# Optimization experiments

Measured on AMD Instinct MI355X. Metric: run time of the kernel, lower is better.

Reference implementation:

```python
import jax, jax.numpy as jnp
import numpy as np

B, T, I, H, C, S = 512, 128, 512, 512, 97, 26  # batch, enc_len, input, hidden, classes, num_steps


def setup_inputs() -> dict:
    key = jax.random.key(0)
    ks = jax.random.split(key, 12)
    s = 0.05
    d = {}
    d["batch_H"] = jax.random.normal(ks[0], (B, T, I), dtype=jnp.float32)
    d["text"] = jax.random.randint(ks[1], (B, S), 0, C)
    # attention cell params
    d["W_feat"] = jax.random.normal(ks[2], (H, I), dtype=jnp.float32) * s   # feature_projection (no bias)
    d["W_hid"] = jax.random.normal(ks[3], (H, H), dtype=jnp.float32) * s    # hidden_projection
    d["b_hid"] = jnp.zeros((H,), dtype=jnp.float32)
    d["w_score"] = jax.random.normal(ks[4], (H,), dtype=jnp.float32) * s    # attention_score (Linear(H,1), no bias)
    # LSTMCell params, PyTorch gate order [i, f, g, o]
    d["W_ih"] = jax.random.normal(ks[5], (4 * H, I + C), dtype=jnp.float32) * s
    d["W_hh"] = jax.random.normal(ks[6], (4 * H, H), dtype=jnp.float32) * s
    d["b_ih"] = jnp.zeros((4 * H,), dtype=jnp.float32)
    d["b_hh"] = jnp.zeros((4 * H,), dtype=jnp.float32)
    # generator
    d["W_gen"] = jax.random.normal(ks[7], (C, H), dtype=jnp.float32) * s
    d["b_gen"] = jnp.zeros((C,), dtype=jnp.float32)
    return d


def reference(batch_H, text, W_feat, W_hid, b_hid, w_score, W_ih, W_hh, b_ih, b_hh, W_gen, b_gen):
    Bb, Tt, _ = batch_H.shape
    Hh = W_hid.shape[0]
    Cc = W_gen.shape[0]
    # step-invariant: project encoder features once  [B, T, H]
    feat = jnp.einsum('bti,hi->bth', batch_H, W_feat)
    onehots = jax.nn.one_hot(text, Cc, dtype=batch_H.dtype)  # [B, S, C]

    def step(carry, oh):
        h, c = carry
        hp = h @ W_hid.T + b_hid                                     # [B, H]
        e = jnp.einsum('bth,h->bt', jnp.tanh(feat + hp[:, None, :]), w_score)
        alpha = jax.nn.softmax(e, axis=1)                            # [B, T]
        ctx = jnp.einsum('bt,bti->bi', alpha, batch_H)               # [B, I]
        x = jnp.concatenate([ctx, oh], axis=1)                       # [B, I+C]
        gates = x @ W_ih.T + b_ih + h @ W_hh.T + b_hh                # [B, 4H]
        i_g, f_g, g_g, o_g = jnp.split(gates, 4, axis=1)
        c2 = jax.nn.sigmoid(f_g) * c + jax.nn.sigmoid(i_g) * jnp.tanh(g_g)
        h2 = jax.nn.sigmoid(o_g) * jnp.tanh(c2)
        return (h2, c2), h2

    init = (jnp.zeros((Bb, Hh), dtype=batch_H.dtype), jnp.zeros((Bb, Hh), dtype=batch_H.dtype))
    _, hs = jax.lax.scan(step, init, jnp.swapaxes(onehots, 0, 1))    # hs: [S, B, H]
    out_h = jnp.swapaxes(hs, 0, 1)                                   # [B, S, H]
    probs = out_h @ W_gen.T + b_gen                                  # [B, S, C]
    return probs
```

## Files before the change

### kernel.cpp

```cpp
#include <hip/hip_runtime.h>
#include <hip/hip_bf16.h>
#include <stdint.h>
#include <stddef.h>

typedef __bf16 bf16;
typedef __bf16 v8bf __attribute__((ext_vector_type(8)));
typedef float  v4f  __attribute__((ext_vector_type(4)));

#define B_ 512
#define T_ 128
#define I_ 512
#define H_ 512
#define C_ 97
#define S_ 26

__device__ __forceinline__ void async_copy16(void* lds, const void* g) {
  __builtin_amdgcn_global_load_lds((__attribute__((address_space(1))) void*)g,
                                   (__attribute__((address_space(3))) void*)lds,
                                   16, 0, 0);
}

__device__ __forceinline__ float fast_tanh(float x) {
  float e = __expf(2.0f * x);
  return fmaf(-2.0f, __builtin_amdgcn_rcpf(e + 1.0f), 1.0f);
}
__device__ __forceinline__ float fast_sigmoid(float x) {
  float t = __expf(-x);
  return __builtin_amdgcn_rcpf(1.0f + t);
}

__device__ __forceinline__ void zero_acc(v4f acc[4][4]) {
  v4f z = {0.f, 0.f, 0.f, 0.f};
#pragma unroll
  for (int i = 0; i < 4; ++i)
#pragma unroll
    for (int j = 0; j < 4; ++j) acc[i][j] = z;
}

template <int KTOT>
__device__ __forceinline__ void mm_db32(const bf16* aRow0, const bf16* aRow1,
                                        const bf16* bRow0, const bf16* bRow1,
                                        bf16* As, bf16* Bs, int tid,
                                        v4f acc[4][4]) {
  constexpr int NT = KTOT / 32;
  const int wave = tid >> 6, lane = tid & 63;
  const int wr = (wave >> 1) * 64, wc = (wave & 1) * 64;
  const int fr = lane & 15, fq = lane >> 4;
  const int s0 = tid * 8;
  const int aBase = (wr + fr) * 32 + fq * 8;
  const int bBase = (wc + fr) * 32 + fq * 8;
  async_copy16(As + s0, aRow0);
  async_copy16(As + s0 + 2048, aRow1);
  async_copy16(Bs + s0, bRow0);
  async_copy16(Bs + s0 + 2048, bRow1);
  __syncthreads();
#pragma unroll 2
  for (int t = 0; t < NT; ++t) {
    const int cb = (t & 1) << 12;
    if (t + 1 < NT) {
      const int nb = 4096 - cb;
      const int kk = (t + 1) * 32;
      async_copy16(As + nb + s0, aRow0 + kk);
      async_copy16(As + nb + s0 + 2048, aRow1 + kk);
      async_copy16(Bs + nb + s0, bRow0 + kk);
      async_copy16(Bs + nb + s0 + 2048, bRow1 + kk);
    }
    v8bf av[4], bv[4];
#pragma unroll
    for (int i = 0; i < 4; ++i) av[i] = *(const v8bf*)(As + cb + aBase + i * 512);
#pragma unroll
    for (int j = 0; j < 4; ++j) bv[j] = *(const v8bf*)(Bs + cb + bBase + j * 512);
#pragma unroll
    for (int i = 0; i < 4; ++i) {
#pragma unroll
      for (int j = 0; j < 4; ++j) {
        acc[i][j] = __builtin_amdgcn_mfma_f32_16x16x32_bf16(av[i], bv[j], acc[i][j], 0, 0, 0);
      }
    }
    __syncthreads();
  }
}

template <int KTOT>
__device__ __forceinline__ void mm_db64(const bf16* aRow0, const bf16* aRow1,
                                        const bf16* bRow0, const bf16* bRow1,
                                        bf16* As, bf16* Bs, int tid,
                                        v4f acc[4][4]) {
  constexpr int NT = KTOT / 64;
  const int wave = tid >> 6, lane = tid & 63;
  const int wr = (wave >> 1) * 64, wc = (wave & 1) * 64;
  const int fr = lane & 15, fq = lane >> 4;
  const int s0 = tid * 8;
  const int aBase = (wr + fr) * 32 + fq * 8;
  const int bBase = (wc + fr) * 32 + fq * 8;
#define STAGE64(buf, kk)                                          \
  do {                                                            \
    async_copy16(As + (buf) + s0, aRow0 + (kk));                  \
    async_copy16(As + (buf) + s0 + 2048, aRow1 + (kk));           \
    async_copy16(As + (buf) + s0 + 4096, aRow0 + (kk) + 32);      \
    async_copy16(As + (buf) + s0 + 6144, aRow1 + (kk) + 32);      \
    async_copy16(Bs + (buf) + s0, bRow0 + (kk));                  \
    async_copy16(Bs + (buf) + s0 + 2048, bRow1 + (kk));           \
    async_copy16(Bs + (buf) + s0 + 4096, bRow0 + (kk) + 32);      \
    async_copy16(Bs + (buf) + s0 + 6144, bRow1 + (kk) + 32);      \
  } while (0)
  STAGE64(0, 0);
  __syncthreads();
#pragma unroll 2
  for (int t = 0; t < NT; ++t) {
    const int cb = (t & 1) << 13;
    if (t + 1 < NT) STAGE64(8192 - cb, (t + 1) * 64);
#pragma unroll
    for (int ks = 0; ks < 2; ++ks) {
      const int sb = cb + ks * 4096;
      v8bf av[4], bv[4];
#pragma unroll
      for (int i = 0; i < 4; ++i) av[i] = *(const v8bf*)(As + sb + aBase + i * 512);
#pragma unroll
      for (int j = 0; j < 4; ++j) bv[j] = *(const v8bf*)(Bs + sb + bBase + j * 512);
#pragma unroll
      for (int i = 0; i < 4; ++i) {
#pragma unroll
        for (int j = 0; j < 4; ++j) {
          acc[i][j] = __builtin_amdgcn_mfma_f32_16x16x32_bf16(av[i], bv[j], acc[i][j], 0, 0, 0);
        }
      }
    }
    __syncthreads();
  }
#undef STAGE64
}

template <int KTOT>
__device__ __forceinline__ void mm_reg_f32a(const float* aR0, const float* aR1,
                                            const bf16* bRow0, const bf16* bRow1,
                                            bf16* As, bf16* Bs, int tid,
                                            v4f acc[4][4]) {
  const int wave = tid >> 6, lane = tid & 63;
  const int wr = (wave >> 1) * 64, wc = (wave & 1) * 64;
  const int fr = lane & 15, fq = lane >> 4;
  bf16* a_s0 = As + tid * 8;
  bf16* a_s1 = As + (tid + 256) * 8;
  bf16* b_s0 = Bs + tid * 8;
  bf16* b_s1 = Bs + (tid + 256) * 8;
  const bf16* aF[4];
  const bf16* bF[4];
#pragma unroll
  for (int i = 0; i < 4; ++i) {
    aF[i] = As + (wr + i * 16 + fr) * 32 + fq * 8;
    bF[i] = Bs + (wc + i * 16 + fr) * 32 + fq * 8;
  }
  for (int kk = 0; kk < KTOT; kk += 32) {
    v8bf va0, va1;
    const float* p0 = aR0 + kk;
    const float* p1 = aR1 + kk;
    v4f f00 = ((const v4f*)p0)[0], f01 = ((const v4f*)p0)[1];
    v4f f10 = ((const v4f*)p1)[0], f11 = ((const v4f*)p1)[1];
#pragma unroll
    for (int j = 0; j < 4; ++j) {
      va0[j] = (bf16)f00[j]; va0[j + 4] = (bf16)f01[j];
      va1[j] = (bf16)f10[j]; va1[j + 4] = (bf16)f11[j];
    }
    v8bf vb0 = *(const v8bf*)(bRow0 + kk);
    v8bf vb1 = *(const v8bf*)(bRow1 + kk);
    __syncthreads();
    *(v8bf*)a_s0 = va0;
    *(v8bf*)a_s1 = va1;
    *(v8bf*)b_s0 = vb0;
    *(v8bf*)b_s1 = vb1;
    __syncthreads();
    v8bf av[4], bv[4];
#pragma unroll
    for (int i = 0; i < 4; ++i) av[i] = *(const v8bf*)aF[i];
#pragma unroll
    for (int j = 0; j < 4; ++j) bv[j] = *(const v8bf*)bF[j];
#pragma unroll
    for (int i = 0; i < 4; ++i) {
#pragma unroll
      for (int j = 0; j < 4; ++j) {
        acc[i][j] = __builtin_amdgcn_mfma_f32_16x16x32_bf16(av[i], bv[j], acc[i][j], 0, 0, 0);
      }
    }
  }
  __syncthreads();
}

__global__ void k_cvt(const float* __restrict__ src, bf16* __restrict__ dst, int n) {
  int i = (blockIdx.x * 256 + threadIdx.x) * 4;
  if (i + 3 < n) {
    v4f f = *(const v4f*)(src + i);
#pragma unroll
    for (int j = 0; j < 4; ++j) dst[i + j] = (bf16)f[j];
  }
}

__global__ void k_repack(const float* __restrict__ Wih, const float* __restrict__ Whh,
                         bf16* __restrict__ Wcat) {
  int n = blockIdx.x;
  int t = threadIdx.x;
#pragma unroll
  for (int j = 0; j < 4; ++j) {
    int k = t * 4 + j;
    float v = (k < 512) ? Wih[(size_t)n * 609 + k] : Whh[(size_t)n * 512 + (k - 512)];
    Wcat[(size_t)n * 1024 + k] = (bf16)v;
  }
}

__global__ void k_prep_gen(const float* __restrict__ Wg, bf16* __restrict__ Wgen16) {
  int row = blockIdx.x;
  int t = threadIdx.x;
#pragma unroll
  for (int j = 0; j < 2; ++j) {
    int k = t * 2 + j;
    float v = (row < C_) ? Wg[(size_t)row * 512 + k] : 0.0f;
    Wgen16[(size_t)row * 512 + k] = (bf16)v;
  }
}

__global__ void k_prep_oht(const float* __restrict__ Wih, float* __restrict__ OHT) {
  int n = blockIdx.x * 256 + threadIdx.x;
  const float* src = Wih + (size_t)n * 609 + 512;
  for (int c = 0; c < C_; ++c) OHT[(size_t)c * 2048 + n] = src[c];
}


__global__ __launch_bounds__(256, 3) void k_feat16(const bf16* __restrict__ A,
                                                   const bf16* __restrict__ Bw,
                                                   bf16* __restrict__ F) {
  __shared__ bf16 As[2 * 4096];
  __shared__ bf16 Bs[2 * 4096];
  const int tid = threadIdx.x;
  const int m0 = blockIdx.x * 128, n0 = blockIdx.y * 128;
  const int r0 = tid >> 2, k0 = (tid & 3) * 8;
  const bf16* aRow0 = A + (size_t)(m0 + r0) * 512 + k0;
  const bf16* aRow1 = A + (size_t)(m0 + r0 + 64) * 512 + k0;
  const bf16* bRow0 = Bw + (size_t)(n0 + r0) * 512 + k0;
  const bf16* bRow1 = Bw + (size_t)(n0 + r0 + 64) * 512 + k0;
  v4f acc[4][4];
  zero_acc(acc);
  mm_db32<512>(aRow0, aRow1, bRow0, bRow1, As, Bs, tid, acc);
  const int wave = tid >> 6, lane = tid & 63;
  const int wr = (wave >> 1) * 64, wc = (wave & 1) * 64;
  const int fr = lane & 15, fq = lane >> 4;
#pragma unroll
  for (int i = 0; i < 4; ++i) {
#pragma unroll
    for (int j = 0; j < 4; ++j) {
      int col = n0 + wc + j * 16 + fr;
#pragma unroll
      for (int r = 0; r < 4; ++r) {
        int row = m0 + wr + i * 16 + fq * 4 + r;
        F[(size_t)row * 512 + col] = (bf16)acc[i][j][r];
      }
    }
  }
}

__global__ __launch_bounds__(256, 2) void k_feat32(const float* __restrict__ A,
                                                   const bf16* __restrict__ Bw,
                                                   bf16* __restrict__ F) {
  __shared__ bf16 As[128 * 32];
  __shared__ bf16 Bs[128 * 32];
  const int tid = threadIdx.x;
  const int m0 = blockIdx.x * 128, n0 = blockIdx.y * 128;
  const int r0 = tid >> 2, k0 = (tid & 3) * 8;
  const float* aRow0 = A + (size_t)(m0 + r0) * 512 + k0;
  const float* aRow1 = A + (size_t)(m0 + r0 + 64) * 512 + k0;
  const bf16* bRow0 = Bw + (size_t)(n0 + r0) * 512 + k0;
  const bf16* bRow1 = Bw + (size_t)(n0 + r0 + 64) * 512 + k0;
  v4f acc[4][4];
  zero_acc(acc);
  mm_reg_f32a<512>(aRow0, aRow1, bRow0, bRow1, As, Bs, tid, acc);
  const int wave = tid >> 6, lane = tid & 63;
  const int wr = (wave >> 1) * 64, wc = (wave & 1) * 64;
  const int fr = lane & 15, fq = lane >> 4;
#pragma unroll
  for (int i = 0; i < 4; ++i) {
#pragma unroll
    for (int j = 0; j < 4; ++j) {
      int col = n0 + wc + j * 16 + fr;
#pragma unroll
      for (int r = 0; r < 4; ++r) {
        int row = m0 + wr + i * 16 + fq * 4 + r;
        F[(size_t)row * 512 + col] = (bf16)acc[i][j][r];
      }
    }
  }
}

__global__ __launch_bounds__(256) void k_hp(const bf16* __restrict__ xb_cur,
                                            const bf16* __restrict__ Whid16,
                                            const float* __restrict__ b_hid,
                                            float* __restrict__ P) {
  __shared__ bf16 As[2 * 2048];
  __shared__ bf16 Bs[2 * 2048];
  const int tid = threadIdx.x, wave = tid >> 6, lane = tid & 63;
  const int m0 = blockIdx.x * 64, n0 = blockIdx.y * 64;
  const int r0 = tid >> 2, k0 = (tid & 3) * 8;
  const bf16* aRow = xb_cur + (size_t)(m0 + r0) * 1024 + 512 + k0;
  const bf16* bRow = Whid16 + (size_t)(n0 + r0) * 512 + k0;
  const int s0 = tid * 8;
  const int fr = lane & 15, fq = lane >> 4;
  const int aBase = fr * 32 + fq * 8;
  const int bBase = (wave * 16 + fr) * 32 + fq * 8;
  v4f acc[4];
  v4f z = {0.f, 0.f, 0.f, 0.f};
#pragma unroll
  for (int i = 0; i < 4; ++i) acc[i] = z;
  async_copy16(As + s0, aRow);
  async_copy16(Bs + s0, bRow);
  __syncthreads();
#pragma unroll 2
  for (int t = 0; t < 16; ++t) {
    const int cb = (t & 1) << 11;
    if (t + 1 < 16) {
      const int nb = 2048 - cb;
      const int kk = (t + 1) * 32;
      async_copy16(As + nb + s0, aRow + kk);
      async_copy16(Bs + nb + s0, bRow + kk);
    }
    v8bf bv = *(const v8bf*)(Bs + cb + bBase);
#pragma unroll
    for (int i = 0; i < 4; ++i) {
      acc[i] = __builtin_amdgcn_mfma_f32_16x16x32_bf16(*(const v8bf*)(As + cb + aBase + i * 512),
                                                       bv, acc[i], 0, 0, 0);
    }
    __syncthreads();
  }
  const int col = n0 + wave * 16 + fr;
  const float bh = b_hid[col];
#pragma unroll
  for (int i = 0; i < 4; ++i) {
#pragma unroll
    for (int r = 0; r < 4; ++r) {
      int row = m0 + i * 16 + fq * 4 + r;
      P[(size_t)row * 512 + col] = acc[i][r] + bh;
    }
  }
}

template <bool CTX16>
__global__ __launch_bounds__(512, 4) void k_attn(const bf16* __restrict__ F,
                                                 const float* __restrict__ P,
                                                 const float* __restrict__ w_score,
                                                 const void* __restrict__ bHv,
                                                 bf16* __restrict__ xb_cur) {
  const int b = blockIdx.x;
  const int tid = threadIdx.x, wave = tid >> 6, lane = tid & 63;
  __shared__ float e_s[T_];
  __shared__ float alpha_s[T_];
  __shared__ float red[8][I_];
  float Pv[8], Wv[8];
  {
    const float* p = P + (size_t)b * H_ + lane * 8;
#pragma unroll
    for (int j = 0; j < 8; ++j) Pv[j] = p[j];
    const float* w = w_score + lane * 8;
#pragma unroll
    for (int j = 0; j < 8; ++j) Wv[j] = w[j];
  }
  const bf16* Fb = F + (size_t)b * T_ * H_ + lane * 8;
#pragma unroll
  for (int t = wave; t < T_; t += 32) {
    v8bf r0 = *(const v8bf*)(Fb + (size_t)t * H_);
    v8bf r1 = *(const v8bf*)(Fb + (size_t)(t + 8) * H_);
    v8bf r2 = *(const v8bf*)(Fb + (size_t)(t + 16) * H_);
    v8bf r3 = *(const v8bf*)(Fb + (size_t)(t + 24) * H_);
    float a0 = 0.f, a1 = 0.f, a2 = 0.f, a3 = 0.f;
#pragma unroll
    for (int j = 0; j < 8; ++j) a0 = fmaf(Wv[j], fast_tanh((float)r0[j] + Pv[j]), a0);
#pragma unroll
    for (int j = 0; j < 8; ++j) a1 = fmaf(Wv[j], fast_tanh((float)r1[j] + Pv[j]), a1);
#pragma unroll
    for (int j = 0; j < 8; ++j) a2 = fmaf(Wv[j], fast_tanh((float)r2[j] + Pv[j]), a2);
#pragma unroll
    for (int j = 0; j < 8; ++j) a3 = fmaf(Wv[j], fast_tanh((float)r3[j] + Pv[j]), a3);
#pragma unroll
    for (int off = 32; off; off >>= 1) {
      a0 += __shfl_xor(a0, off, 64);
      a1 += __shfl_xor(a1, off, 64);
      a2 += __shfl_xor(a2, off, 64);
      a3 += __shfl_xor(a3, off, 64);
    }
    if (lane == 0) {
      e_s[t] = a0; e_s[t + 8] = a1; e_s[t + 16] = a2; e_s[t + 24] = a3;
    }
  }
  __syncthreads();
  if (wave == 0) {
    float e0 = e_s[lane], e1 = e_s[lane + 64];
    float m = fmaxf(e0, e1);
#pragma unroll
    for (int off = 32; off; off >>= 1) m = fmaxf(m, __shfl_xor(m, off, 64));
    float x0 = __expf(e0 - m), x1 = __expf(e1 - m);
    float ssum = x0 + x1;
#pragma unroll
    for (int off = 32; off; off >>= 1) ssum += __shfl_xor(ssum, off, 64);
    float inv = __builtin_amdgcn_rcpf(ssum);
    alpha_s[lane] = x0 * inv;
    alpha_s[lane + 64] = x1 * inv;
  }
  __syncthreads();
  const int i0 = lane * 8;
  float c[8];
#pragma unroll
  for (int j = 0; j < 8; ++j) c[j] = 0.f;
  if (CTX16) {
    const bf16* hb = (const bf16*)bHv + (size_t)b * T_ * I_ + i0;
#pragma unroll
    for (int t = wave; t < T_; t += 32) {
      float aa0 = alpha_s[t], aa1 = alpha_s[t + 8];
      float aa2 = alpha_s[t + 16], aa3 = alpha_s[t + 24];
      v8bf p0 = *(const v8bf*)(hb + (size_t)t * I_);
      v8bf p1 = *(const v8bf*)(hb + (size_t)(t + 8) * I_);
      v8bf p2 = *(const v8bf*)(hb + (size_t)(t + 16) * I_);
      v8bf p3 = *(const v8bf*)(hb + (size_t)(t + 24) * I_);
#pragma unroll
      for (int j = 0; j < 8; ++j) {
        c[j] = fmaf(aa0, (float)p0[j], c[j]);
        c[j] = fmaf(aa1, (float)p1[j], c[j]);
        c[j] = fmaf(aa2, (float)p2[j], c[j]);
        c[j] = fmaf(aa3, (float)p3[j], c[j]);
      }
    }
  } else {
    const float* hf = (const float*)bHv + (size_t)b * T_ * I_ + i0;
#pragma unroll
    for (int t = wave; t < T_; t += 32) {
      float aa0 = alpha_s[t], aa1 = alpha_s[t + 8];
      float aa2 = alpha_s[t + 16], aa3 = alpha_s[t + 24];
      const float* p0 = hf + (size_t)t * I_;
      const float* p1 = hf + (size_t)(t + 8) * I_;
      const float* p2 = hf + (size_t)(t + 16) * I_;
      const float* p3 = hf + (size_t)(t + 24) * I_;
      v4f q00 = ((const v4f*)p0)[0], q01 = ((const v4f*)p0)[1];
      v4f q10 = ((const v4f*)p1)[0], q11 = ((const v4f*)p1)[1];
      v4f q20 = ((const v4f*)p2)[0], q21 = ((const v4f*)p2)[1];
      v4f q30 = ((const v4f*)p3)[0], q31 = ((const v4f*)p3)[1];
#pragma unroll
      for (int j = 0; j < 4; ++j) {
        c[j]     = fmaf(aa0, q00[j], c[j]);
        c[j + 4] = fmaf(aa0, q01[j], c[j + 4]);
        c[j]     = fmaf(aa1, q10[j], c[j]);
        c[j + 4] = fmaf(aa1, q11[j], c[j + 4]);
        c[j]     = fmaf(aa2, q20[j], c[j]);
        c[j + 4] = fmaf(aa2, q21[j], c[j + 4]);
        c[j]     = fmaf(aa3, q30[j], c[j]);
        c[j + 4] = fmaf(aa3, q31[j], c[j + 4]);
      }
    }
  }
#pragma unroll
  for (int j = 0; j < 8; ++j) red[wave][i0 + j] = c[j];
  __syncthreads();
  {
    int i = tid;
    float s = red[0][i] + red[1][i] + red[2][i] + red[3][i] +
              red[4][i] + red[5][i] + red[6][i] + red[7][i];
    xb_cur[(size_t)b * 1024 + i] = (bf16)s;
  }
}

__global__ __launch_bounds__(256, 2) void k_gates(const bf16* __restrict__ xb_cur,
                                                  const bf16* __restrict__ Wcat,
                                                  const float* __restrict__ OHT,
                                                  const float* __restrict__ b_ih,
                                                  const float* __restrict__ b_hh,
                                                  const int* __restrict__ text,
                                                  float* __restrict__ c_state,
                                                  bf16* __restrict__ out_h,
                                                  bf16* __restrict__ xb_nxt, int s) {
  __shared__ union {
    struct { bf16 A[2 * 8192]; bf16 Bv[2 * 8192]; } st;
    float Cs[128 * 132];
  } sm;
  const int tid = threadIdx.x;
  const int m0 = blockIdx.x * 128;
  const int j0 = blockIdx.y * 32;
  const int r0 = tid >> 2, k0 = (tid & 3) * 8;
  const int nw0 = (r0 >> 5) * 512 + j0 + (r0 & 31);
  const int nw1 = (((r0 + 64) >> 5)) * 512 + j0 + ((r0 + 64) & 31);
  const bf16* aRow0 = xb_cur + (size_t)(m0 + r0) * 1024 + k0;
  const bf16* aRow1 = xb_cur + (size_t)(m0 + r0 + 64) * 1024 + k0;
  const bf16* bRow0 = Wcat + (size_t)nw0 * 1024 + k0;
  const bf16* bRow1 = Wcat + (size_t)nw1 * 1024 + k0;
  v4f acc[4][4];
  zero_acc(acc);
  mm_db64<1024>(aRow0, aRow1, bRow0, bRow1, sm.st.A, sm.st.Bv, tid, acc);
  const int wave = tid >> 6, lane = tid & 63;
  const int wr = (wave >> 1) * 64, wc = (wave & 1) * 64;
  const int fr = lane & 15, fq = lane >> 4;
  int tcv[4][4];
#pragma unroll
  for (int i = 0; i < 4; ++i) {
#pragma unroll
    for (int r = 0; r < 4; ++r) {
      tcv[i][r] = text[(size_t)(m0 + wr + i * 16 + fq * 4 + r) * S_ + s];
    }
  }
#pragma unroll
  for (int j = 0; j < 4; ++j) {
    int cl = wc + j * 16 + fr;
    int nw = (cl >> 5) * 512 + j0 + (cl & 31);
    float bias = b_ih[nw] + b_hh[nw];
    const float* oh = OHT + nw;
#pragma unroll
    for (int i = 0; i < 4; ++i) {
#pragma unroll
      for (int r = 0; r < 4; ++r) {
        int rl = wr + i * 16 + fq * 4 + r;
        sm.Cs[rl * 132 + cl] = acc[i][j][r] + bias + oh[(size_t)tcv[i][r] * 2048];
      }
    }
  }
  __syncthreads();
#pragma unroll
  for (int it = 0; it < 16; ++it) {
    int idx = tid + it * 256;
    int r = idx >> 5, q = idx & 31;
    float ig = sm.Cs[r * 132 + q];
    float fg = sm.Cs[r * 132 + 32 + q];
    float gg = sm.Cs[r * 132 + 64 + q];
    float og = sm.Cs[r * 132 + 96 + q];
    size_t cix = (size_t)(m0 + r) * 512 + j0 + q;
    float c2 = fast_sigmoid(fg) * c_state[cix] + fast_sigmoid(ig) * fast_tanh(gg);
    float h2 = fast_sigmoid(og) * fast_tanh(c2);
    c_state[cix] = c2;
    bf16 hb = (bf16)h2;
    xb_nxt[(size_t)(m0 + r) * 1024 + 512 + j0 + q] = hb;
    out_h[((size_t)(m0 + r) * S_ + s) * 512 + j0 + q] = hb;
  }
}

__global__ __launch_bounds__(256, 2) void k_gen(const bf16* __restrict__ out_h,
                                                const bf16* __restrict__ Wgen16,
                                                const float* __restrict__ b_gen,
                                                float* __restrict__ out) {
  __shared__ bf16 As[2 * 8192];
  __shared__ bf16 Bs[2 * 8192];
  const int tid = threadIdx.x;
  const int m0 = blockIdx.x * 128;
  const int r0 = tid >> 2, k0 = (tid & 3) * 8;
  const bf16* aRow0 = out_h + (size_t)(m0 + r0) * 512 + k0;
  const bf16* aRow1 = out_h + (size_t)(m0 + r0 + 64) * 512 + k0;
  const bf16* bRow0 = Wgen16 + (size_t)r0 * 512 + k0;
  const bf16* bRow1 = Wgen16 + (size_t)(r0 + 64) * 512 + k0;
  v4f acc[4][4];
  zero_acc(acc);
  mm_db64<512>(aRow0, aRow1, bRow0, bRow1, As, Bs, tid, acc);
  const int wave = tid >> 6, lane = tid & 63;
  const int wr = (wave >> 1) * 64, wc = (wave & 1) * 64;
  const int fr = lane & 15, fq = lane >> 4;
#pragma unroll
  for (int i = 0; i < 4; ++i) {
#pragma unroll
    for (int j = 0; j < 4; ++j) {
      int col = wc + j * 16 + fr;
      if (col < C_) {
        float bg = b_gen[col];
#pragma unroll
        for (int r = 0; r < 4; ++r) {
          int row = m0 + wr + i * 16 + fq * 4 + r;
          out[(size_t)row * C_ + col] = acc[i][j][r] + bg;
        }
      }
    }
  }
}

extern "C" void kernel_launch(void* const* d_in, const int* in_sizes, int n_in,
                              void* d_out, int out_size, void* d_ws, size_t ws_size,
                              hipStream_t stream) {
  (void)in_sizes; (void)n_in; (void)out_size;
  const float* batch_H = (const float*)d_in[0];
  const int*   text    = (const int*)d_in[1];
  const float* W_feat  = (const float*)d_in[2];
  const float* W_hid   = (const float*)d_in[3];
  const float* b_hid   = (const float*)d_in[4];
  const float* w_score = (const float*)d_in[5];
  const float* W_ih    = (const float*)d_in[6];
  const float* W_hh    = (const float*)d_in[7];
  const float* b_ih    = (const float*)d_in[8];
  const float* b_hh    = (const float*)d_in[9];
  const float* W_gen   = (const float*)d_in[10];
  const float* b_gen   = (const float*)d_in[11];
  float* out = (float*)d_out;

  char* ws = (char*)d_ws;
  bf16*  F       = (bf16*)(ws);
  bf16*  out_h   = (bf16*)(ws + 67108864);
  float* P       = (float*)(ws + 80740352);
  bf16*  xb0     = (bf16*)(ws + 81788928);
  bf16*  xb1     = (bf16*)(ws + 82837504);
  float* c_state = (float*)(ws + 83886080);
  bf16*  Wcat    = (bf16*)(ws + 84934656);
  bf16*  Wf16    = (bf16*)(ws + 89128960);
  bf16*  Whid16  = (bf16*)(ws + 89653248);
  bf16*  Wgen16  = (bf16*)(ws + 90177536);
  float* OHT     = (float*)(ws + 90308608);
  bf16*  bH16    = (bf16*)(ws + 91357184);
  const bool useBH16 = (ws_size >= (size_t)158466048);

  bf16* xb[2] = {xb0, xb1};

  hipMemsetAsync(xb0, 0, (size_t)512 * 1024 * 2, stream);
  hipMemsetAsync(c_state, 0, (size_t)512 * 512 * 4, stream);

  k_cvt<<<dim3(256), 256, 0, stream>>>(W_feat, Wf16, 512 * 512);
  k_cvt<<<dim3(256), 256, 0, stream>>>(W_hid, Whid16, 512 * 512);
  k_repack<<<dim3(2048), 256, 0, stream>>>(W_ih, W_hh, Wcat);
  k_prep_gen<<<dim3(128), 256, 0, stream>>>(W_gen, Wgen16);
  k_prep_oht<<<dim3(8), 256, 0, stream>>>(W_ih, OHT);

  if (useBH16) {
    k_cvt<<<dim3(32768), 256, 0, stream>>>(batch_H, bH16, B_ * T_ * I_);
    k_feat16<<<dim3(512, 4), 256, 0, stream>>>(bH16, Wf16, F);
  } else {
    k_feat32<<<dim3(512, 4), 256, 0, stream>>>(batch_H, Wf16, F);
  }

  for (int s = 0; s < S_; ++s) {
    bf16* cur = xb[s & 1];
    bf16* nxt = xb[(s + 1) & 1];
    k_hp<<<dim3(8, 8), 256, 0, stream>>>(cur, Whid16, b_hid, P);
    if (useBH16) {
      k_attn<true><<<dim3(512), 512, 0, stream>>>(F, P, w_score, bH16, cur);
    } else {
      k_attn<false><<<dim3(512), 512, 0, stream>>>(F, P, w_score, batch_H, cur);
    }
    k_gates<<<dim3(4, 16), 256, 0, stream>>>(cur, Wcat, OHT, b_ih, b_hh, text,
                                             c_state, out_h, nxt, s);
  }
  k_gen<<<dim3(104, 1), 256, 0, stream>>>(out_h, Wgen16, b_gen, out);
}
```

Baseline: 1.659 ms.

## Replace double-buffered GEMM loops with 4-slot, prefetch-distance-2 pipeline using vmcnt waits

Replaces the double-buffered GEMM mainloops (mm_db32/mm_db64) with a single quad-buffered routine that keeps two K-tiles in flight. Each iteration waits with s_waitcnt vmcnt plus a single barrier, where the old loop used a full __syncthreads after every tile. This is meant to hide more global-load latency in the feat, hidden-projection, gates and generator GEMMs. In exchange the kernels use more LDS, occupancy hints are relaxed, and k_gates drops from K-step 64 to 32 and needs an extra sync before its epilogue reuses shared memory.

```diff
diff --git a/kernel.cpp b/kernel.cpp
--- a/kernel.cpp
+++ b/kernel.cpp
@@ -37,8 +37,15 @@
     for (int j = 0; j < 4; ++j) acc[i][j] = z;
 }
 
+#define WAITBAR(N)                                             \
+  do {                                                         \
+    asm volatile("s_waitcnt vmcnt(" #N ")" ::: "memory");      \
+    __builtin_amdgcn_s_barrier();                              \
+    __builtin_amdgcn_sched_barrier(0);                         \
+  } while (0)
+
 template <int KTOT>
-__device__ __forceinline__ void mm_db32(const bf16* aRow0, const bf16* aRow1,
+__device__ __forceinline__ void mm_qb32(const bf16* aRow0, const bf16* aRow1,
                                         const bf16* bRow0, const bf16* bRow1,
                                         bf16* As, bf16* Bs, int tid,
                                         v4f acc[4][4]) {
@@ -47,29 +54,33 @@
   const int wr = (wave >> 1) * 64, wc = (wave & 1) * 64;
   const int fr = lane & 15, fq = lane >> 4;
   const int s0 = tid * 8;
-  const int aBase = (wr + fr) * 32 + fq * 8;
-  const int bBase = (wc + fr) * 32 + fq * 8;
-  async_copy16(As + s0, aRow0);
-  async_copy16(As + s0 + 2048, aRow1);
-  async_copy16(Bs + s0, bRow0);
-  async_copy16(Bs + s0 + 2048, bRow1);
-  __syncthreads();
-#pragma unroll 2
+  const int aB = (wr + fr) * 32 + fq * 8;
+  const int bB = (wc + fr) * 32 + fq * 8;
+#define STG32(bi, kk)                                   \
+  do {                                                  \
+    const int o = (bi) * 4096 + s0;                     \
+    async_copy16(As + o, aRow0 + (kk));                 \
+    async_copy16(As + o + 2048, aRow1 + (kk));          \
+    async_copy16(Bs + o, bRow0 + (kk));                 \
+    async_copy16(Bs + o + 2048, bRow1 + (kk));          \
+  } while (0)
+  STG32(0, 0);
+  STG32(1, 32);
   for (int t = 0; t < NT; ++t) {
-    const int cb = (t & 1) << 12;
-    if (t + 1 < NT) {
-      const int nb = 4096 - cb;
-      const int kk = (t + 1) * 32;
-      async_copy16(As + nb + s0, aRow0 + kk);
-      async_copy16(As + nb + s0 + 2048, aRow1 + kk);
-      async_copy16(Bs + nb + s0, bRow0 + kk);
-      async_copy16(Bs + nb + s0 + 2048, bRow1 + kk);
-    }
+    if (t + 2 < NT) {
+      STG32((t + 2) & 3, (t + 2) * 32);
+      WAITBAR(8);
+    } else if (t + 1 < NT) {
+      WAITBAR(4);
+    } else {
+      WAITBAR(0);
+    }
+    const int cb = (t & 3) * 4096;
     v8bf av[4], bv[4];
 #pragma unroll
-    for (int i = 0; i < 4; ++i) av[i] = *(const v8bf*)(As + cb + aBase + i * 512);
-#pragma unroll
-    for (int j = 0; j < 4; ++j) bv[j] = *(const v8bf*)(Bs + cb + bBase + j * 512);
+    for (int i = 0; i < 4; ++i) av[i] = *(const v8bf*)(As + cb + aB + i * 512);
+#pragma unroll
+    for (int j = 0; j < 4; ++j) bv[j] = *(const v8bf*)(Bs + cb + bB + j * 512);
 #pragma unroll
     for (int i = 0; i < 4; ++i) {
 #pragma unroll
@@ -77,58 +88,8 @@
         acc[i][j] = __builtin_amdgcn_mfma_f32_16x16x32_bf16(av[i], bv[j], acc[i][j], 0, 0, 0);
       }
     }
-    __syncthreads();
-  }
-}
-
-template <int KTOT>
-__device__ __forceinline__ void mm_db64(const bf16* aRow0, const bf16* aRow1,
-                                        const bf16* bRow0, const bf16* bRow1,
-                                        bf16* As, bf16* Bs, int tid,
-                                        v4f acc[4][4]) {
-  constexpr int NT = KTOT / 64;
-  const int wave = tid >> 6, lane = tid & 63;
-  const int wr = (wave >> 1) * 64, wc = (wave & 1) * 64;
-  const int fr = lane & 15, fq = lane >> 4;
-  const int s0 = tid * 8;
-  const int aBase = (wr + fr) * 32 + fq * 8;
-  const int bBase = (wc + fr) * 32 + fq * 8;
-#define STAGE64(buf, kk)                                          \
-  do {                                                            \
-    async_copy16(As + (buf) + s0, aRow0 + (kk));                  \
-    async_copy16(As + (buf) + s0 + 2048, aRow1 + (kk));           \
-    async_copy16(As + (buf) + s0 + 4096, aRow0 + (kk) + 32);      \
-    async_copy16(As + (buf) + s0 + 6144, aRow1 + (kk) + 32);      \
-    async_copy16(Bs + (buf) + s0, bRow0 + (kk));                  \
-    async_copy16(Bs + (buf) + s0 + 2048, bRow1 + (kk));           \
-    async_copy16(Bs + (buf) + s0 + 4096, bRow0 + (kk) + 32);      \
-    async_copy16(Bs + (buf) + s0 + 6144, bRow1 + (kk) + 32);      \
-  } while (0)
-  STAGE64(0, 0);
-  __syncthreads();
-#pragma unroll 2
-  for (int t = 0; t < NT; ++t) {
-    const int cb = (t & 1) << 13;
-    if (t + 1 < NT) STAGE64(8192 - cb, (t + 1) * 64);
-#pragma unroll
-    for (int ks = 0; ks < 2; ++ks) {
-      const int sb = cb + ks * 4096;
-      v8bf av[4], bv[4];
-#pragma unroll
-      for (int i = 0; i < 4; ++i) av[i] = *(const v8bf*)(As + sb + aBase + i * 512);
-#pragma unroll
-      for (int j = 0; j < 4; ++j) bv[j] = *(const v8bf*)(Bs + sb + bBase + j * 512);
-#pragma unroll
-      for (int i = 0; i < 4; ++i) {
-#pragma unroll
-        for (int j = 0; j < 4; ++j) {
-          acc[i][j] = __builtin_amdgcn_mfma_f32_16x16x32_bf16(av[i], bv[j], acc[i][j], 0, 0, 0);
-        }
-      }
-    }
-    __syncthreads();
-  }
-#undef STAGE64
+  }
+#undef STG32
 }
 
 template <int KTOT>
@@ -224,11 +185,11 @@
 }
 
 
-__global__ __launch_bounds__(256, 3) void k_feat16(const bf16* __restrict__ A,
+__global__ __launch_bounds__(256, 2) void k_feat16(const bf16* __restrict__ A,
                                                    const bf16* __restrict__ Bw,
                                                    bf16* __restrict__ F) {
-  __shared__ bf16 As[2 * 4096];
-  __shared__ bf16 Bs[2 * 4096];
+  __shared__ bf16 As[4 * 4096];
+  __shared__ bf16 Bs[4 * 4096];
   const int tid = threadIdx.x;
   const int m0 = blockIdx.x * 128, n0 = blockIdx.y * 128;
   const int r0 = tid >> 2, k0 = (tid & 3) * 8;
@@ -238,7 +199,7 @@
   const bf16* bRow1 = Bw + (size_t)(n0 + r0 + 64) * 512 + k0;
   v4f acc[4][4];
   zero_acc(acc);
-  mm_db32<512>(aRow0, aRow1, bRow0, bRow1, As, Bs, tid, acc);
+  mm_qb32<512>(aRow0, aRow1, bRow0, bRow1, As, Bs, tid, acc);
   const int wave = tid >> 6, lane = tid & 63;
   const int wr = (wave >> 1) * 64, wc = (wave & 1) * 64;
   const int fr = lane & 15, fq = lane >> 4;
@@ -292,8 +253,8 @@
                                             const bf16* __restrict__ Whid16,
                                             const float* __restrict__ b_hid,
                                             float* __restrict__ P) {
-  __shared__ bf16 As[2 * 2048];
-  __shared__ bf16 Bs[2 * 2048];
+  __shared__ bf16 As[4 * 4096];
+  __shared__ bf16 Bs[4 * 4096];
   const int tid = threadIdx.x, wave = tid >> 6, lane = tid & 63;
   const int m0 = blockIdx.x * 64, n0 = blockIdx.y * 64;
   const int r0 = tid >> 2, k0 = (tid & 3) * 8;
@@ -301,32 +262,45 @@
   const bf16* bRow = Whid16 + (size_t)(n0 + r0) * 512 + k0;
   const int s0 = tid * 8;
   const int fr = lane & 15, fq = lane >> 4;
-  const int aBase = fr * 32 + fq * 8;
-  const int bBase = (wave * 16 + fr) * 32 + fq * 8;
+  const int aB = fr * 32 + fq * 8;
+  const int bB = (wave * 16 + fr) * 32 + fq * 8;
   v4f acc[4];
   v4f z = {0.f, 0.f, 0.f, 0.f};
 #pragma unroll
   for (int i = 0; i < 4; ++i) acc[i] = z;
-  async_copy16(As + s0, aRow);
-  async_copy16(Bs + s0, bRow);
-  __syncthreads();
-#pragma unroll 2
-  for (int t = 0; t < 16; ++t) {
-    const int cb = (t & 1) << 11;
-    if (t + 1 < 16) {
-      const int nb = 2048 - cb;
-      const int kk = (t + 1) * 32;
-      async_copy16(As + nb + s0, aRow + kk);
-      async_copy16(Bs + nb + s0, bRow + kk);
-    }
-    v8bf bv = *(const v8bf*)(Bs + cb + bBase);
-#pragma unroll
-    for (int i = 0; i < 4; ++i) {
-      acc[i] = __builtin_amdgcn_mfma_f32_16x16x32_bf16(*(const v8bf*)(As + cb + aBase + i * 512),
-                                                       bv, acc[i], 0, 0, 0);
-    }
-    __syncthreads();
-  }
+#define STGH(bi, kk)                                    \
+  do {                                                  \
+    const int o = (bi) * 4096 + s0;                     \
+    async_copy16(As + o, aRow + (kk));                  \
+    async_copy16(As + o + 2048, aRow + (kk) + 32);      \
+    async_copy16(Bs + o, bRow + (kk));                  \
+    async_copy16(Bs + o + 2048, bRow + (kk) + 32);      \
+  } while (0)
+  STGH(0, 0);
+  STGH(1, 64);
+  constexpr int NT = 8;
+  for (int t = 0; t < NT; ++t) {
+    if (t + 2 < NT) {
+      STGH((t + 2) & 3, (t + 2) * 64);
+      WAITBAR(8);
+    } else if (t + 1 < NT) {
+      WAITBAR(4);
+    } else {
+      WAITBAR(0);
+    }
+    const int cb = (t & 3) * 4096;
+#pragma unroll
+    for (int ks = 0; ks < 2; ++ks) {
+      const int sb = cb + ks * 2048;
+      v8bf bv = *(const v8bf*)(Bs + sb + bB);
+#pragma unroll
+      for (int i = 0; i < 4; ++i) {
+        acc[i] = __builtin_amdgcn_mfma_f32_16x16x32_bf16(*(const v8bf*)(As + sb + aB + i * 512),
+                                                         bv, acc[i], 0, 0, 0);
+      }
+    }
+  }
+#undef STGH
   const int col = n0 + wave * 16 + fr;
   const float bh = b_hid[col];
 #pragma unroll
@@ -461,17 +435,17 @@
   }
 }
 
-__global__ __launch_bounds__(256, 2) void k_gates(const bf16* __restrict__ xb_cur,
-                                                  const bf16* __restrict__ Wcat,
-                                                  const float* __restrict__ OHT,
-                                                  const float* __restrict__ b_ih,
-                                                  const float* __restrict__ b_hh,
-                                                  const int* __restrict__ text,
-                                                  float* __restrict__ c_state,
-                                                  bf16* __restrict__ out_h,
-                                                  bf16* __restrict__ xb_nxt, int s) {
+__global__ __launch_bounds__(256) void k_gates(const bf16* __restrict__ xb_cur,
+                                               const bf16* __restrict__ Wcat,
+                                               const float* __restrict__ OHT,
+                                               const float* __restrict__ b_ih,
+                                               const float* __restrict__ b_hh,
+                                               const int* __restrict__ text,
+                                               float* __restrict__ c_state,
+                                               bf16* __restrict__ out_h,
+                                               bf16* __restrict__ xb_nxt, int s) {
   __shared__ union {
-    struct { bf16 A[2 * 8192]; bf16 Bv[2 * 8192]; } st;
+    struct { bf16 A[4 * 4096]; bf16 Bv[4 * 4096]; } st;
     float Cs[128 * 132];
   } sm;
   const int tid = threadIdx.x;
@@ -486,7 +460,8 @@
   const bf16* bRow1 = Wcat + (size_t)nw1 * 1024 + k0;
   v4f acc[4][4];
   zero_acc(acc);
-  mm_db64<1024>(aRow0, aRow1, bRow0, bRow1, sm.st.A, sm.st.Bv, tid, acc);
+  mm_qb32<1024>(aRow0, aRow1, bRow0, bRow1, sm.st.A, sm.st.Bv, tid, acc);
+  __syncthreads();
   const int wave = tid >> 6, lane = tid & 63;
   const int wr = (wave >> 1) * 64, wc = (wave & 1) * 64;
   const int fr = lane & 15, fq = lane >> 4;
@@ -532,12 +507,12 @@
   }
 }
 
-__global__ __launch_bounds__(256, 2) void k_gen(const bf16* __restrict__ out_h,
-                                                const bf16* __restrict__ Wgen16,
-                                                const float* __restrict__ b_gen,
-                                                float* __restrict__ out) {
-  __shared__ bf16 As[2 * 8192];
-  __shared__ bf16 Bs[2 * 8192];
+__global__ __launch_bounds__(256) void k_gen(const bf16* __restrict__ out_h,
+                                             const bf16* __restrict__ Wgen16,
+                                             const float* __restrict__ b_gen,
+                                             float* __restrict__ out) {
+  __shared__ bf16 As[4 * 4096];
+  __shared__ bf16 Bs[4 * 4096];
   const int tid = threadIdx.x;
   const int m0 = blockIdx.x * 128;
   const int r0 = tid >> 2, k0 = (tid & 3) * 8;
@@ -547,7 +522,7 @@
   const bf16* bRow1 = Wgen16 + (size_t)(r0 + 64) * 512 + k0;
   v4f acc[4][4];
   zero_acc(acc);
-  mm_db64<512>(aRow0, aRow1, bRow0, bRow1, As, Bs, tid, acc);
+  mm_qb32<512>(aRow0, aRow1, bRow0, bRow1, As, Bs, tid, acc);
   const int wave = tid >> 6, lane = tid & 63;
   const int wr = (wave >> 1) * 64, wc = (wave & 1) * 64;
   const int fr = lane & 15, fq = lane >> 4;
```

Measured after the change: 1.535 ms. 1.08x faster.
